# Performance work log

Measured on AMD Instinct MI355X. Metric: run time of the kernel, lower is better.

Reference implementation:

```python
import jax, jax.numpy as jnp
import numpy as np

NUM_HEADS = 12
ALPHA = 4.0
EPS = 1e-6

def safe_pow(x, p):
    # relu(x)**p with grad-safe handling of x<=0 (avoids nan from log(0) in pow grads)
    xp = jnp.where(x > 0, x, 1.0)
    return jnp.where(x > 0, xp ** p, 0.0)

def setup_inputs() -> dict:
    key = jax.random.key(0)
    ks = jax.random.split(key, 9)
    B, N, C = 8, 4096, 768
    Hn, hd, ksz = NUM_HEADS, C // NUM_HEADS, 5
    return {
        "x": jax.random.normal(ks[0], (B, N, C), jnp.float32),
        "Wqg": jax.random.normal(ks[1], (C, 2 * C), jnp.float32) * 0.02,
        "Wkv": jax.random.normal(ks[2], (C, 2 * C), jnp.float32) * 0.02,
        "Wproj": jax.random.normal(ks[3], (C, C), jnp.float32) * 0.02,
        "bproj": jnp.zeros((C,), jnp.float32),
        "dwc_w": jax.random.normal(ks[4], (hd, 1, ksz, ksz), jnp.float32) * 0.05,
        "dwc_b": jnp.zeros((hd,), jnp.float32),
        "power_p": jax.random.normal(ks[5], (1, Hn, 1, hd), jnp.float32) * 0.01,
        "scale_p": jax.random.normal(ks[6], (1, 1, C), jnp.float32) * 0.01,
        "pos_enc": jax.random.normal(ks[7], (1, N, C), jnp.float32) * 0.01,
    }

def reference(x, Wqg, Wkv, Wproj, bproj, dwc_w, dwc_b, power_p, scale_p, pos_enc):
    B, N, C = x.shape
    Hn = NUM_HEADS
    hd = C // Hn
    # q/g projection: [B,N,2C] -> q = [...,0,:], g = [...,1,:]
    qg = (x @ Wqg).reshape(B, N, 2, C)
    q, g = qg[:, :, 0], qg[:, :, 1]
    # k/v projection (sr_ratio == 1)
    kvp = x @ Wkv
    k, v = kvp[..., :C], kvp[..., C:]
    k = k + pos_enc
    scale = jax.nn.softplus(scale_p)            # [1,1,C]
    power = 1.0 + ALPHA * jax.nn.sigmoid(power_p)  # [1,Hn,1,hd]
    q = q / scale
    k = k / scale
    # -> [B,Hn,N,hd]
    q = q.reshape(B, N, Hn, hd).transpose(0, 2, 1, 3)
    k = k.reshape(B, N, Hn, hd).transpose(0, 2, 1, 3)
    v = v.reshape(B, N, Hn, hd).transpose(0, 2, 1, 3)
    q_pos = safe_pow(q, power)
    q_neg = safe_pow(-q, power)
    k_pos = safe_pow(k, power)
    k_neg = safe_pow(-k, power)
    q_sim = jnp.concatenate([q_pos, q_neg], -1)  # [B,Hn,N,2hd]
    q_opp = jnp.concatenate([q_neg, q_pos], -1)
    k_cat = jnp.concatenate([k_pos, k_neg], -1)
    v1, v2 = jnp.split(v, 2, axis=-1)            # [B,Hn,N,hd/2]
    n = N
    inv_n = 1.0 / n
    k_mean = k_cat.mean(axis=2, keepdims=True)   # [B,Hn,1,2hd]
    z_sim = 1.0 / (jnp.einsum('bhnk,bhmk->bhnm', q_sim, k_mean) + EPS)  # [B,Hn,N,1]
    kv1 = jnp.einsum('bhnk,bhnv->bhkv', k_cat, v1) * inv_n
    x_sim = jnp.einsum('bhnk,bhkv->bhnv', q_sim, kv1) * z_sim
    z_opp = 1.0 / (jnp.einsum('bhnk,bhmk->bhnm', q_opp, k_mean) + EPS)
    kv2 = jnp.einsum('bhnk,bhnv->bhkv', k_cat, v2) * inv_n
    x_opp = jnp.einsum('bhnk,bhkv->bhnv', q_opp, kv2) * z_opp
    xa = jnp.concatenate([x_sim, x_opp], -1).transpose(0, 2, 1, 3).reshape(B, N, C)
    # depthwise-conv positional branch on v (head-major channel layout)
    Hs = int(np.sqrt(N))
    v_img = v.reshape(B * Hn, Hs, Hs, hd).transpose(0, 3, 1, 2)  # [B*Hn, hd, Hs, Hs]
    v_conv = jax.lax.conv_general_dilated(
        v_img, dwc_w, (1, 1), 'SAME', feature_group_count=hd,
        dimension_numbers=('NCHW', 'OIHW', 'NCHW')) + dwc_b[None, :, None, None]
    v_pos = v_conv.reshape(B, C, N).transpose(0, 2, 1)  # [B,N,C]
    out = (xa + v_pos) * g
    return out @ Wproj + bproj
```

## Files before the change

kernel.cpp:

```cpp
#include <hip/hip_runtime.h>


typedef _Float16 f16;
typedef __attribute__((ext_vector_type(4))) float f32x4;
typedef __attribute__((ext_vector_type(8))) _Float16 f16x8;
typedef __attribute__((ext_vector_type(4))) _Float16 f16x4;

__device__ __forceinline__ void mfma(f32x4& c, f16x8 a, f16x8 b) {
  c = __builtin_amdgcn_mfma_f32_16x16x32_f16(a, b, c, 0, 0, 0);
}

__device__ __forceinline__ void gload_lds16(const f16* g, f16* l) {
  __builtin_amdgcn_global_load_lds(
      (__attribute__((address_space(1))) void*)g,
      (__attribute__((address_space(3))) void*)l, 16, 0, 0);
}

__device__ __forceinline__ f16x8 relu8(f16x8 v) {
  f16x8 r;
#pragma unroll
  for (int u = 0; u < 8; ++u) r[u] = (v[u] > (f16)0) ? v[u] : (f16)0;
  return r;
}
__device__ __forceinline__ f16x8 nrelu8(f16x8 v) {
  f16x8 r;
#pragma unroll
  for (int u = 0; u < 8; ++u) r[u] = (v[u] < (f16)0) ? (f16)(-v[u]) : (f16)0;
  return r;
}

__global__ void prep_scalars_kernel(const float* __restrict__ scale_p,
                                    const float* __restrict__ power_p,
                                    float* __restrict__ iscale,
                                    float* __restrict__ powr) {
  int c = blockIdx.x * 256 + threadIdx.x;
  if (c < 768) {
    float sp = scale_p[c];
    float s = (sp > 20.f) ? sp : log1pf(__expf(sp));
    iscale[c] = 1.f / s;
    powr[c] = 1.f + 4.f / (1.f + __expf(-power_p[c]));
  }
}

__global__ __launch_bounds__(256) void cast_x_kernel(const float* __restrict__ x,
                                                     f16* __restrict__ xblk) {
  __shared__ f16 tile[128 * 72];
  const int kb = blockIdx.x, mt = blockIdx.y, t = threadIdx.x;
  const float* xp = x + (size_t)mt * 128 * 768 + kb * 64;
#pragma unroll
  for (int it = 0; it < 8; ++it) {
    int idx = it * 256 + t;
    int row = idx >> 4, kc4 = (idx & 15) * 4;
    f32x4 v = *(const f32x4*)(xp + (size_t)row * 768 + kc4);
    f16x4 h;
    h[0] = (f16)v[0]; h[1] = (f16)v[1]; h[2] = (f16)v[2]; h[3] = (f16)v[3];
    *(f16x4*)(tile + row * 72 + kc4) = h;
  }
  __syncthreads();
  f16* op = xblk + (size_t)mt * 98304 + kb * 8192;
#pragma unroll
  for (int it = 0; it < 4; ++it) {
    int c = it * 256 + t;
    int kchunk = c >> 7, m = c & 127;
    f16x4 lo = *(const f16x4*)(tile + m * 72 + kchunk * 8);
    f16x4 hi = *(const f16x4*)(tile + m * 72 + kchunk * 8 + 4);
    *(f16x4*)(op + c * 8) = lo;
    *(f16x4*)(op + c * 8 + 4) = hi;
  }
}

__global__ __launch_bounds__(256) void transpose_w_kernel(const float* __restrict__ W,
                                                          f16* __restrict__ outblk,
                                                          int Cc, int col_off) {
  __shared__ float tile[32][33];
  const int c0 = blockIdx.x * 32, r0 = blockIdx.y * 32, t = threadIdx.x;
#pragma unroll
  for (int it = 0; it < 4; ++it) {
    int rr = it * 8 + (t >> 5), cc = t & 31;
    tile[rr][cc] = W[(size_t)(r0 + rr) * Cc + c0 + cc];
  }
  __syncthreads();
  if (t < 128) {
    int cl = t >> 2, rb = t & 3;
    int cg = col_off + c0 + cl;
    int rg = r0 + rb * 8;
    f16x4 v0, v1;
#pragma unroll
    for (int u = 0; u < 4; ++u) v0[u] = (f16)tile[rb * 8 + u][cl];
#pragma unroll
    for (int u = 0; u < 4; ++u) v1[u] = (f16)tile[rb * 8 + 4 + u][cl];
    size_t base = (size_t)(cg >> 7) * 98304 + (size_t)(rg >> 3) * 1024 +
                  (size_t)(cg & 127) * 8;
    *(f16x4*)(outblk + base) = v0;
    *(f16x4*)(outblk + base + 4) = v1;
  }
}

template <int MODE>
__global__ __launch_bounds__(256) void gemm_kernel(
    const f16* __restrict__ Ablk, const f16* __restrict__ Bblk,
    const float* __restrict__ powr, const float* __restrict__ iscale,
    const float* __restrict__ pos_enc, const float* __restrict__ bproj,
    f16* __restrict__ qpow, f16* __restrict__ gbuf, f16* __restrict__ kpow,
    f16* __restrict__ vt, float* __restrict__ outp) {
  __shared__ f16 As[8192];
  __shared__ f16 Bs[8192];
  const int t = threadIdx.x;
  const int wave = t >> 6, lane = t & 63;
  const int c16 = lane & 15, q = lane >> 4;
  const int flat = blockIdx.y * gridDim.x + blockIdx.x;
  const int chunk = (int)(gridDim.x * gridDim.y) >> 3;
  const int sw = (flat & 7) * chunk + (flat >> 3);
  const int ntile = sw % (int)gridDim.x;
  const int mtile = sw / (int)gridDim.x;
  const int mwave = (wave >> 1) * 64, nwave = (wave & 1) * 64;
  const f16* Ap = Ablk + (size_t)mtile * 98304;
  const f16* Bp = Bblk + (size_t)ntile * 98304;

  f32x4 acc[4][4];
#pragma unroll
  for (int i = 0; i < 4; ++i)
#pragma unroll
    for (int j = 0; j < 4; ++j) acc[i][j] = (f32x4){0.f, 0.f, 0.f, 0.f};

  for (int k0 = 0; k0 < 768; k0 += 64) {
#pragma unroll
    for (int r = 0; r < 4; ++r) {
      const int cl = r * 256 + t;
      const int cu = r * 256 + wave * 64;
      gload_lds16(Ap + (size_t)k0 * 128 + (size_t)cl * 8,
                  As + (size_t)cu * 8);
      gload_lds16(Bp + (size_t)k0 * 128 + (size_t)cl * 8,
                  Bs + (size_t)cu * 8);
    }
    __syncthreads();
#pragma unroll
    for (int s = 0; s < 2; ++s) {
      f16x8 af[4], bfr[4];
#pragma unroll
      for (int i = 0; i < 4; ++i) {
        af[i] = *(const f16x8*)(As + (s * 4 + q) * 1024 + (mwave + i * 16 + c16) * 8);
        bfr[i] = *(const f16x8*)(Bs + (s * 4 + q) * 1024 + (nwave + i * 16 + c16) * 8);
      }
#pragma unroll
      for (int i = 0; i < 4; ++i)
#pragma unroll
        for (int j = 0; j < 4; ++j) mfma(acc[i][j], af[i], bfr[j]);
    }
    __syncthreads();
  }

  if (MODE == 0) {
    const int sec = ntile / 6;
    const int cbase = ntile * 128 - sec * 768;
    const int b = mtile >> 5;
    const int nim0 = (mtile & 31) * 128;
#pragma unroll
    for (int i = 0; i < 4; ++i) {
      const int nloc = nim0 + mwave + i * 16 + q * 4;
#pragma unroll
      for (int j = 0; j < 4; ++j) {
        const int c = cbase + nwave + j * 16 + c16;
        const int h = c >> 6, d = c & 63;
        const int bh = b * 12 + h;
        if (sec == 0) {
          const float p = powr[c], isc = iscale[c];
          const size_t qb2 = (size_t)bh * 262144 + (size_t)(nloc >> 7) * 8192;
          const int dpo = (d >> 3) * 1024 + (d & 7);
#pragma unroll
          for (int r2 = 0; r2 < 4; ++r2) {
            float val = acc[i][j][r2] * isc;
            float av = fabsf(val);
            float e = (av > 0.f) ? exp2f(p * __log2f(av)) : 0.f;
            float s = (val > 0.f) ? e : ((val < 0.f) ? -e : 0.f);
            int mrow = (nloc + r2) & 127;
            qpow[qb2 + mrow * 8 + dpo] = (f16)s;
          }
        } else if (sec == 1) {
#pragma unroll
          for (int r2 = 0; r2 < 4; ++r2)
            gbuf[((size_t)bh * 4096 + nloc + r2) * 64 + d] = (f16)acc[i][j][r2];
        } else if (sec == 2) {
          const float p = powr[c], isc = iscale[c];
          f16x4 pk;
#pragma unroll
          for (int r2 = 0; r2 < 4; ++r2) {
            int n = nloc + r2;
            float val = (acc[i][j][r2] + pos_enc[(size_t)n * 768 + c]) * isc;
            float av = fabsf(val);
            float e = (av > 0.f) ? exp2f(p * __log2f(av)) : 0.f;
            pk[r2] = (f16)((val > 0.f) ? e : ((val < 0.f) ? -e : 0.f));
          }
          const size_t kb2 =
              (size_t)bh * 262144 + (size_t)(nloc >> 3) * 512 + (nloc & 7);
          *(f16x4*)(kpow + kb2 + (size_t)d * 8) = pk;
        } else {
          f16x4 vv4;
#pragma unroll
          for (int r2 = 0; r2 < 4; ++r2) vv4[r2] = (f16)acc[i][j][r2];
          *(f16x4*)(vt + (size_t)(bh * 64 + d) * 4096 + nloc) = vv4;
        }
      }
    }
  } else {
#pragma unroll
    for (int i = 0; i < 4; ++i) {
      const int tok0 = mtile * 128 + mwave + i * 16 + q * 4;
#pragma unroll
      for (int j = 0; j < 4; ++j) {
        const int col = ntile * 128 + nwave + j * 16 + c16;
        const float bb = bproj[col];
#pragma unroll
        for (int r2 = 0; r2 < 4; ++r2)
          outp[(size_t)(tok0 + r2) * 768 + col] = acc[i][j][r2] + bb;
      }
    }
  }
}

__global__ __launch_bounds__(256) void kv_kernel(const f16* __restrict__ kpow,
                                                 const f16* __restrict__ vt,
                                                 float* __restrict__ kvp,
                                                 float* __restrict__ ksp) {
  __shared__ f16 Ks[8192];
  __shared__ f16 Vs[4096];
  __shared__ float rp[256], rn[256];
  const int bh = blockIdx.x, split = blockIdx.y, t = threadIdx.x;
  const int wave = t >> 6, lane = t & 63;
  const int c16 = lane & 15, q = lane >> 4;
  const f16* kb = kpow + (size_t)bh * 262144;
  const f16* vb = vt + (size_t)bh * 64 * 4096;
  f32x4 acc[4][2];
#pragma unroll
  for (int i = 0; i < 4; ++i)
#pragma unroll
    for (int j = 0; j < 2; ++j) acc[i][j] = (f32x4){0.f, 0.f, 0.f, 0.f};
  float sp = 0.f, sn = 0.f;

  const int n_beg = split * 1024, n_end = n_beg + 1024;
  for (int n0 = n_beg; n0 < n_end; n0 += 64) {
    f16x8 kr[2], vr[2];
#pragma unroll
    for (int r = 0; r < 2; ++r)
      kr[r] = *(const f16x8*)(kb + (size_t)n0 * 64 + (size_t)(r * 256 + t) * 8);
#pragma unroll
    for (int r = 0; r < 2; ++r) {
      int cc = r * 256 + t;
      int vv = cc >> 3, nc = cc & 7;
      vr[r] = *(const f16x8*)(vb + (size_t)vv * 4096 + n0 + nc * 8);
    }
#pragma unroll
    for (int r = 0; r < 2; ++r)
#pragma unroll
      for (int u = 0; u < 8; ++u) {
        float f = (float)kr[r][u];
        sp += (f > 0.f) ? f : 0.f;
        sn += (f < 0.f) ? -f : 0.f;
      }
    __syncthreads();
#pragma unroll
    for (int r = 0; r < 2; ++r) {
      int cp = r * 256 + t;
      int nch = cp >> 6, d = cp & 63;
      *(f16x8*)(Ks + (size_t)(nch * 1024 + d * 8)) = relu8(kr[r]);
      *(f16x8*)(Ks + (size_t)(nch * 1024 + (d + 64) * 8)) = nrelu8(kr[r]);
    }
#pragma unroll
    for (int r = 0; r < 2; ++r) {
      int cc = r * 256 + t;
      int vv = cc >> 3, nc = cc & 7;
      *(f16x8*)(Vs + (size_t)(nc * 64 + (vv ^ nc)) * 8) = vr[r];
    }
    __syncthreads();
#pragma unroll
    for (int s = 0; s < 2; ++s) {
      f16x8 af[4], bf2[2];
#pragma unroll
      for (int i = 0; i < 4; ++i) {
        int m = i * 16 + c16, nc2 = s * 4 + q;
        af[i] = *(const f16x8*)(Vs + (nc2 * 64 + (m ^ nc2)) * 8);
      }
#pragma unroll
      for (int j = 0; j < 2; ++j)
        bf2[j] = *(const f16x8*)(Ks + ((s * 4 + q) * 128 + wave * 32 + j * 16 + c16) * 8);
#pragma unroll
      for (int i = 0; i < 4; ++i)
#pragma unroll
        for (int j = 0; j < 2; ++j) mfma(acc[i][j], af[i], bf2[j]);
    }
    __syncthreads();
  }
  float* kvb = kvp + (size_t)(bh * 4 + split) * 8192;
#pragma unroll
  for (int i = 0; i < 4; ++i)
#pragma unroll
    for (int j = 0; j < 2; ++j) {
      int kk = wave * 32 + j * 16 + c16;
      int vv0 = i * 16 + q * 4;
#pragma unroll
      for (int r2 = 0; r2 < 4; ++r2)
        kvb[(size_t)(vv0 + r2) * 128 + kk] = acc[i][j][r2];
    }
  rp[t] = sp; rn[t] = sn;
  __syncthreads();
  if (t < 64) {
    float* ko = ksp + (size_t)(bh * 4 + split) * 128;
    ko[t] = rp[t] + rp[t + 64] + rp[t + 128] + rp[t + 192];
    ko[64 + t] = rn[t] + rn[t + 64] + rn[t + 128] + rn[t + 192];
  }
}

__global__ void bx_kernel(const float* __restrict__ kvp,
                          const float* __restrict__ ksp, f16* __restrict__ bxt) {
  const int bh = blockIdx.x, kk = threadIdx.x;
  const float inv_n = 1.f / 4096.f;
  const float* kv0 = kvp + (size_t)bh * 4 * 8192;
  const float* ks0 = ksp + (size_t)bh * 4 * 128;
  f16* ob = bxt + (size_t)bh * 80 * 128;
  for (int nn = 0; nn < 32; ++nn) {
    float v = kv0[nn * 128 + kk] + kv0[8192 + nn * 128 + kk] +
              kv0[16384 + nn * 128 + kk] + kv0[24576 + nn * 128 + kk];
    ob[nn * 128 + kk] = (f16)(v * inv_n);
  }
  const int kx = kk ^ 64;
  for (int nn = 32; nn < 64; ++nn) {
    float v = kv0[nn * 128 + kx] + kv0[8192 + nn * 128 + kx] +
              kv0[16384 + nn * 128 + kx] + kv0[24576 + nn * 128 + kx];
    ob[nn * 128 + kk] = (f16)(v * inv_n);
  }
  float s0 = ks0[kk] + ks0[128 + kk] + ks0[256 + kk] + ks0[384 + kk];
  ob[64 * 128 + kk] = (f16)(s0 * inv_n);
  float s1 = ks0[kx] + ks0[128 + kx] + ks0[256 + kx] + ks0[384 + kx];
  ob[65 * 128 + kk] = (f16)(s1 * inv_n);
  for (int nn = 66; nn < 80; ++nn) ob[nn * 128 + kk] = (f16)0.f;
}

__global__ __launch_bounds__(256) void conv_kernel(const f16* __restrict__ vt,
                                                   const float* __restrict__ w,
                                                   const float* __restrict__ bias,
                                                   f16* __restrict__ vpos) {
  __shared__ float img[68 * 69];
  const int blk = blockIdx.x;
  const int d = blk & 63, bh = blk >> 6;
  const f16* src = vt + (size_t)(bh * 64 + d) * 4096;
  for (int i = threadIdx.x; i < 68 * 68; i += 256) {
    int yy = i / 68, xx = i - yy * 68;
    int y = yy - 2, x = xx - 2;
    float val = 0.f;
    if (((unsigned)y < 64u) && ((unsigned)x < 64u)) val = (float)src[y * 64 + x];
    img[yy * 69 + xx] = val;
  }
  float wr[25];
#pragma unroll
  for (int k = 0; k < 25; ++k) wr[k] = w[d * 25 + k];
  const float bb = bias[d];
  __syncthreads();
  f16* dst = vpos + (size_t)(bh * 64 + d) * 4096;
  for (int g4 = threadIdx.x; g4 < 1024; g4 += 256) {
    int y = g4 >> 4, x4 = (g4 & 15) * 4;
    float o0 = bb, o1 = bb, o2 = bb, o3 = bb;
#pragma unroll
    for (int ky = 0; ky < 5; ++ky) {
      const float* row = img + (y + ky) * 69 + x4;
      float r[8];
#pragma unroll
      for (int u = 0; u < 8; ++u) r[u] = row[u];
#pragma unroll
      for (int kx = 0; kx < 5; ++kx) {
        float wv = wr[ky * 5 + kx];
        o0 += r[kx] * wv;
        o1 += r[kx + 1] * wv;
        o2 += r[kx + 2] * wv;
        o3 += r[kx + 3] * wv;
      }
    }
    f16x4 st;
    st[0] = (f16)o0; st[1] = (f16)o1; st[2] = (f16)o2; st[3] = (f16)o3;
    *(f16x4*)(dst + y * 64 + x4) = st;
  }
}

__global__ __launch_bounds__(256) void xa_kernel(
    const f16* __restrict__ qpow, const f16* __restrict__ bxt,
    const f16* __restrict__ vpos, const f16* __restrict__ gbuf,
    f16* __restrict__ pre) {
  __shared__ f16 Qs[16384];
  __shared__ f16 Ps[64 * 134];
  __shared__ float zs[256];
  const int nb = blockIdx.x, bh = blockIdx.y;
  const int b = bh / 12, h = bh % 12;
  const int t = threadIdx.x;
  const int wave = t >> 6, lane = t & 63;
  const int c16 = lane & 15, q = lane >> 4;
  const f16* qb = qpow + (size_t)bh * 262144 + (size_t)nb * 8192;
  f16x8 qr[4];
#pragma unroll
  for (int r = 0; r < 4; ++r)
    qr[r] = *(const f16x8*)(qb + (size_t)(r * 256 + t) * 8);
#pragma unroll
  for (int r = 0; r < 4; ++r) {
    int c = r * 256 + t;
    int dch = c >> 7, row = c & 127;
    *(f16x8*)(Qs + (size_t)(dch * 1024 + row * 8)) = relu8(qr[r]);
    *(f16x8*)(Qs + (size_t)((dch + 8) * 1024 + row * 8)) = nrelu8(qr[r]);
  }
  {
    const f16* vpb = vpos + (size_t)bh * 262144 + (size_t)nb * 128;
#pragma unroll
    for (int it = 0; it < 4; ++it) {
      int idx = it * 256 + t;
      int col = idx >> 4, nc = idx & 15;
      f16x8 v = *(const f16x8*)(vpb + (size_t)col * 4096 + nc * 8);
      *(f16x8*)(Ps + col * 134 + nc * 8) = v;
    }
  }
  __syncthreads();
  f32x4 acc[2][5];
#pragma unroll
  for (int i = 0; i < 2; ++i)
#pragma unroll
    for (int j = 0; j < 5; ++j) acc[i][j] = (f32x4){0.f, 0.f, 0.f, 0.f};
  const f16* bx = bxt + (size_t)bh * 80 * 128;
#pragma unroll
  for (int s = 0; s < 4; ++s) {
    f16x8 af[2], bf5[5];
#pragma unroll
    for (int i = 0; i < 2; ++i)
      af[i] = *(const f16x8*)(Qs + ((s * 4 + q) * 1024 + (wave * 32 + i * 16 + c16) * 8));
#pragma unroll
    for (int j = 0; j < 5; ++j)
      bf5[j] = *(const f16x8*)(bx + (size_t)(j * 16 + c16) * 128 + s * 32 + q * 8);
#pragma unroll
    for (int i = 0; i < 2; ++i)
#pragma unroll
      for (int j = 0; j < 5; ++j) mfma(acc[i][j], af[i], bf5[j]);
  }
  if (c16 < 2) {
#pragma unroll
    for (int i = 0; i < 2; ++i) {
      int mloc = wave * 32 + i * 16 + q * 4;
#pragma unroll
      for (int r2 = 0; r2 < 4; ++r2) zs[(mloc + r2) * 2 + c16] = acc[i][4][r2];
    }
  }
  __syncthreads();
#pragma unroll
  for (int i = 0; i < 2; ++i) {
    const int mbase = wave * 32 + i * 16 + q * 4;
#pragma unroll
    for (int j = 0; j < 4; ++j) {
      const int col = j * 16 + c16;
      const int cch = h * 64 + col;
      const int zsel = col >> 5;
#pragma unroll
      for (int r2 = 0; r2 < 4; ++r2) {
        const int mloc = mbase + r2;
        const int n = nb * 128 + mloc;
        const float den = zs[mloc * 2 + zsel];
        const float xav = acc[i][j][r2] / (den + 1e-6f);
        const float vp = (float)Ps[col * 134 + mloc];
        const float gg = (float)gbuf[((size_t)bh * 4096 + n) * 64 + col];
        const int tok = b * 4096 + n;
        pre[(size_t)(tok >> 7) * 98304 + (size_t)(cch >> 3) * 1024 +
            (tok & 127) * 8 + (cch & 7)] = (f16)((xav + vp) * gg);
      }
    }
  }
}

extern "C" void kernel_launch(void* const* d_in, const int* in_sizes, int n_in,
                              void* d_out, int out_size, void* d_ws, size_t ws_size,
                              hipStream_t stream) {
  const float* x       = (const float*)d_in[0];
  const float* Wqg     = (const float*)d_in[1];
  const float* Wkv     = (const float*)d_in[2];
  const float* Wproj   = (const float*)d_in[3];
  const float* bproj   = (const float*)d_in[4];
  const float* dwc_w   = (const float*)d_in[5];
  const float* dwc_b   = (const float*)d_in[6];
  const float* power_p = (const float*)d_in[7];
  const float* scale_p = (const float*)d_in[8];
  const float* pos_enc = (const float*)d_in[9];
  float* outp = (float*)d_out;

  char* ws = (char*)d_ws;
  constexpr size_t o_qpow = 0;
  constexpr size_t o_kpow = 50331648;
  constexpr size_t o_vt   = 100663296;
  constexpr size_t o_gbuf = 150994944;
  constexpr size_t o_xblk = 201326592;
  constexpr size_t o_wta  = 251658240;
  constexpr size_t o_wtp  = 256376832;
  constexpr size_t o_isc  = 257556480;
  constexpr size_t o_pwr  = 257560576;
  constexpr size_t o_bxt  = 257564672;
  constexpr size_t o_ks   = 259530752;

  f16*   qpow = (f16*)(ws + o_qpow);
  f16*   kpow = (f16*)(ws + o_kpow);
  f16*   vt   = (f16*)(ws + o_vt);
  f16*   gbuf = (f16*)(ws + o_gbuf);
  f16*   xblk = (f16*)(ws + o_xblk);
  f16*   wta  = (f16*)(ws + o_wta);
  f16*   wtp  = (f16*)(ws + o_wtp);
  float* isc  = (float*)(ws + o_isc);
  float* pwr  = (float*)(ws + o_pwr);
  f16*   bxt  = (f16*)(ws + o_bxt);
  float* kvp  = (float*)(ws + o_xblk);
  float* ksp  = (float*)(ws + o_xblk + 12582912);
  f16*   vpos = kpow;
  f16*   pre  = xblk;

  prep_scalars_kernel<<<dim3(3), 256, 0, stream>>>(scale_p, power_p, isc, pwr);
  cast_x_kernel<<<dim3(12, 256), 256, 0, stream>>>(x, xblk);
  transpose_w_kernel<<<dim3(48, 24), 256, 0, stream>>>(Wqg, wta, 1536, 0);
  transpose_w_kernel<<<dim3(48, 24), 256, 0, stream>>>(Wkv, wta, 1536, 1536);
  transpose_w_kernel<<<dim3(24, 24), 256, 0, stream>>>(Wproj, wtp, 768, 0);
  gemm_kernel<0><<<dim3(24, 256), 256, 0, stream>>>(
      xblk, wta, pwr, isc, pos_enc, nullptr, qpow, gbuf, kpow, vt, nullptr);
  kv_kernel<<<dim3(96, 4), 256, 0, stream>>>(kpow, vt, kvp, ksp);
  bx_kernel<<<96, 128, 0, stream>>>(kvp, ksp, bxt);
  conv_kernel<<<6144, 256, 0, stream>>>(vt, dwc_w, dwc_b, vpos);
  xa_kernel<<<dim3(32, 96), 256, 0, stream>>>(qpow, bxt, vpos, gbuf, pre);
  gemm_kernel<1><<<dim3(6, 256), 256, 0, stream>>>(
      pre, wtp, nullptr, nullptr, nullptr, bproj, nullptr, nullptr, nullptr,
      nullptr, outp);
}
```

Baseline: 701.2 us.

## Double-buffer GEMM LDS staging with larger 512-thread tiles

Restructures both GEMM kernels to use 512-thread blocks with larger output tiles (256x256 for the QKV projection, 256x128 for the output projection). Global-to-LDS loads are double-buffered in dynamic shared memory with explicit vmcnt waits and barriers, and MFMA blocks run under raised wave priority. The aim is to overlap memory staging with matrix math and raise operand reuse per tile. In exchange it uses much more LDS (128KB/96KB), which lowers occupancy, and it drops the grid swizzle for L2 locality.

```diff
diff --git a/kernel.cpp b/kernel.cpp
--- a/kernel.cpp
+++ b/kernel.cpp
@@ -97,79 +97,119 @@
 }
 
 template <int MODE>
-__global__ __launch_bounds__(256) void gemm_kernel(
+__global__ __launch_bounds__(512) void gemm_kernel(
     const f16* __restrict__ Ablk, const f16* __restrict__ Bblk,
     const float* __restrict__ powr, const float* __restrict__ iscale,
     const float* __restrict__ pos_enc, const float* __restrict__ bproj,
     f16* __restrict__ qpow, f16* __restrict__ gbuf, f16* __restrict__ kpow,
     f16* __restrict__ vt, float* __restrict__ outp) {
-  __shared__ f16 As[8192];
-  __shared__ f16 Bs[8192];
+  constexpr int NW    = (MODE == 0) ? 4 : 2;
+  constexpr int MREP  = (MODE == 0) ? 8 : 4;
+  constexpr int BCOLT = (MODE == 0) ? 2 : 1;
+  constexpr int A_H   = 16384;
+  constexpr int STR   = A_H + BCOLT * 8192;
+  extern __shared__ f16 smem[];
   const int t = threadIdx.x;
-  const int wave = t >> 6, lane = t & 63;
+  const int wid = t >> 6, lane = t & 63;
   const int c16 = lane & 15, q = lane >> 4;
-  const int flat = blockIdx.y * gridDim.x + blockIdx.x;
-  const int chunk = (int)(gridDim.x * gridDim.y) >> 3;
-  const int sw = (flat & 7) * chunk + (flat >> 3);
-  const int ntile = sw % (int)gridDim.x;
-  const int mtile = sw / (int)gridDim.x;
-  const int mwave = (wave >> 1) * 64, nwave = (wave & 1) * 64;
-  const f16* Ap = Ablk + (size_t)mtile * 98304;
-  const f16* Bp = Bblk + (size_t)ntile * 98304;
-
-  f32x4 acc[4][4];
-#pragma unroll
-  for (int i = 0; i < 4; ++i)
+  const int mtile = blockIdx.x, ntile = blockIdx.y;
+  const int wm = wid / NW, wn = wid % NW;
+  const f16* Ap = Ablk + (size_t)mtile * 196608;
+  const f16* Bp = Bblk + (size_t)ntile * (BCOLT * 98304);
+  const int ahalf = (MODE == 0) ? wm : (wm >> 1);
+  const int rbase = (MODE == 0) ? 0 : (wm & 1) * 64;
+  const int bhalf = (MODE == 0) ? (wn >> 1) : 0;
+  const int cbase = (MODE == 0) ? (wn & 1) * 64 : wn * 64;
+
+  auto STAGE = [&](int buf, int k0) {
+    const size_t gk = (size_t)k0 * 128;
+#pragma unroll
+    for (int h = 0; h < 2; ++h)
+#pragma unroll
+      for (int r = 0; r < 2; ++r)
+        gload_lds16(Ap + h * 98304 + gk + (size_t)(r * 512 + t) * 8,
+                    smem + buf * STR + h * 8192 + (r * 512 + wid * 64) * 8);
+#pragma unroll
+    for (int h = 0; h < BCOLT; ++h)
+#pragma unroll
+      for (int r = 0; r < 2; ++r)
+        gload_lds16(Bp + h * 98304 + gk + (size_t)(r * 512 + t) * 8,
+                    smem + buf * STR + A_H + h * 8192 + (r * 512 + wid * 64) * 8);
+  };
+
+  f32x4 acc[MREP][4];
+#pragma unroll
+  for (int i = 0; i < MREP; ++i)
 #pragma unroll
     for (int j = 0; j < 4; ++j) acc[i][j] = (f32x4){0.f, 0.f, 0.f, 0.f};
 
-  for (int k0 = 0; k0 < 768; k0 += 64) {
-#pragma unroll
-    for (int r = 0; r < 4; ++r) {
-      const int cl = r * 256 + t;
-      const int cu = r * 256 + wave * 64;
-      gload_lds16(Ap + (size_t)k0 * 128 + (size_t)cl * 8,
-                  As + (size_t)cu * 8);
-      gload_lds16(Bp + (size_t)k0 * 128 + (size_t)cl * 8,
-                  Bs + (size_t)cu * 8);
-    }
-    __syncthreads();
-#pragma unroll
-    for (int s = 0; s < 2; ++s) {
-      f16x8 af[4], bfr[4];
-#pragma unroll
-      for (int i = 0; i < 4; ++i) {
-        af[i] = *(const f16x8*)(As + (s * 4 + q) * 1024 + (mwave + i * 16 + c16) * 8);
-        bfr[i] = *(const f16x8*)(Bs + (s * 4 + q) * 1024 + (nwave + i * 16 + c16) * 8);
-      }
-#pragma unroll
-      for (int i = 0; i < 4; ++i)
-#pragma unroll
-        for (int j = 0; j < 4; ++j) mfma(acc[i][j], af[i], bfr[j]);
-    }
-    __syncthreads();
+  STAGE(0, 0);
+  STAGE(1, 64);
+  if constexpr (MODE == 0) asm volatile("s_waitcnt vmcnt(8)");
+  else                     asm volatile("s_waitcnt vmcnt(6)");
+  __builtin_amdgcn_sched_barrier(0);
+  __builtin_amdgcn_s_barrier();
+  __builtin_amdgcn_sched_barrier(0);
+
+  for (int j = 0; j < 12; ++j) {
+    const int cur = j & 1;
+    const f16* A_ = smem + cur * STR + ahalf * 8192;
+    const f16* B_ = smem + cur * STR + A_H + bhalf * 8192;
+#pragma unroll
+    for (int s2 = 0; s2 < 2; ++s2) {
+      f16x8 af[MREP], bf[4];
+      const int kc = (s2 * 4 + q) * 1024;
+#pragma unroll
+      for (int mi = 0; mi < MREP; ++mi)
+        af[mi] = *(const f16x8*)(A_ + kc + (rbase + mi * 16 + c16) * 8);
+#pragma unroll
+      for (int ni = 0; ni < 4; ++ni)
+        bf[ni] = *(const f16x8*)(B_ + kc + (cbase + ni * 16 + c16) * 8);
+      __builtin_amdgcn_s_setprio(1);
+#pragma unroll
+      for (int mi = 0; mi < MREP; ++mi)
+#pragma unroll
+        for (int ni = 0; ni < 4; ++ni) mfma(acc[mi][ni], af[mi], bf[ni]);
+      __builtin_amdgcn_s_setprio(0);
+    }
+    if (j < 11) {
+      asm volatile("s_waitcnt lgkmcnt(0)");
+      __builtin_amdgcn_sched_barrier(0);
+      __builtin_amdgcn_s_barrier();
+      __builtin_amdgcn_sched_barrier(0);
+      if (j < 10) {
+        STAGE(cur, (j + 2) * 64);
+        if constexpr (MODE == 0) asm volatile("s_waitcnt vmcnt(8)");
+        else                     asm volatile("s_waitcnt vmcnt(6)");
+      } else {
+        asm volatile("s_waitcnt vmcnt(0)");
+      }
+      __builtin_amdgcn_sched_barrier(0);
+      __builtin_amdgcn_s_barrier();
+      __builtin_amdgcn_sched_barrier(0);
+    }
   }
 
   if (MODE == 0) {
-    const int sec = ntile / 6;
-    const int cbase = ntile * 128 - sec * 768;
-    const int b = mtile >> 5;
-    const int nim0 = (mtile & 31) * 128;
-#pragma unroll
-    for (int i = 0; i < 4; ++i) {
-      const int nloc = nim0 + mwave + i * 16 + q * 4;
-#pragma unroll
-      for (int j = 0; j < 4; ++j) {
-        const int c = cbase + nwave + j * 16 + c16;
-        const int h = c >> 6, d = c & 63;
+    const int sec = ntile / 3;
+    const int csb = (ntile - sec * 3) * 256;
+    const int b = mtile >> 4;
+    const int nim0 = (mtile & 15) * 256;
+#pragma unroll
+    for (int mi = 0; mi < MREP; ++mi) {
+      const int nloc = nim0 + wm * 128 + mi * 16 + q * 4;
+#pragma unroll
+      for (int ni = 0; ni < 4; ++ni) {
+        const int cs = csb + wn * 64 + ni * 16 + c16;
+        const int h = cs >> 6, d = cs & 63;
         const int bh = b * 12 + h;
         if (sec == 0) {
-          const float p = powr[c], isc = iscale[c];
+          const float p = powr[cs], isc = iscale[cs];
           const size_t qb2 = (size_t)bh * 262144 + (size_t)(nloc >> 7) * 8192;
           const int dpo = (d >> 3) * 1024 + (d & 7);
 #pragma unroll
           for (int r2 = 0; r2 < 4; ++r2) {
-            float val = acc[i][j][r2] * isc;
+            float val = acc[mi][ni][r2] * isc;
             float av = fabsf(val);
             float e = (av > 0.f) ? exp2f(p * __log2f(av)) : 0.f;
             float s = (val > 0.f) ? e : ((val < 0.f) ? -e : 0.f);
@@ -179,14 +219,14 @@
         } else if (sec == 1) {
 #pragma unroll
           for (int r2 = 0; r2 < 4; ++r2)
-            gbuf[((size_t)bh * 4096 + nloc + r2) * 64 + d] = (f16)acc[i][j][r2];
+            gbuf[((size_t)bh * 4096 + nloc + r2) * 64 + d] = (f16)acc[mi][ni][r2];
         } else if (sec == 2) {
-          const float p = powr[c], isc = iscale[c];
+          const float p = powr[cs], isc = iscale[cs];
           f16x4 pk;
 #pragma unroll
           for (int r2 = 0; r2 < 4; ++r2) {
             int n = nloc + r2;
-            float val = (acc[i][j][r2] + pos_enc[(size_t)n * 768 + c]) * isc;
+            float val = (acc[mi][ni][r2] + pos_enc[(size_t)n * 768 + cs]) * isc;
             float av = fabsf(val);
             float e = (av > 0.f) ? exp2f(p * __log2f(av)) : 0.f;
             pk[r2] = (f16)((val > 0.f) ? e : ((val < 0.f) ? -e : 0.f));
@@ -197,22 +237,22 @@
         } else {
           f16x4 vv4;
 #pragma unroll
-          for (int r2 = 0; r2 < 4; ++r2) vv4[r2] = (f16)acc[i][j][r2];
+          for (int r2 = 0; r2 < 4; ++r2) vv4[r2] = (f16)acc[mi][ni][r2];
           *(f16x4*)(vt + (size_t)(bh * 64 + d) * 4096 + nloc) = vv4;
         }
       }
     }
   } else {
 #pragma unroll
-    for (int i = 0; i < 4; ++i) {
-      const int tok0 = mtile * 128 + mwave + i * 16 + q * 4;
-#pragma unroll
-      for (int j = 0; j < 4; ++j) {
-        const int col = ntile * 128 + nwave + j * 16 + c16;
+    for (int mi = 0; mi < MREP; ++mi) {
+      const int tok0 = mtile * 256 + wm * 64 + mi * 16 + q * 4;
+#pragma unroll
+      for (int ni = 0; ni < 4; ++ni) {
+        const int col = ntile * 128 + wn * 64 + ni * 16 + c16;
         const float bb = bproj[col];
 #pragma unroll
         for (int r2 = 0; r2 < 4; ++r2)
-          outp[(size_t)(tok0 + r2) * 768 + col] = acc[i][j][r2] + bb;
+          outp[(size_t)(tok0 + r2) * 768 + col] = acc[mi][ni][r2] + bb;
       }
     }
   }
@@ -494,7 +534,6 @@
   constexpr size_t o_isc  = 257556480;
   constexpr size_t o_pwr  = 257560576;
   constexpr size_t o_bxt  = 257564672;
-  constexpr size_t o_ks   = 259530752;
 
   f16*   qpow = (f16*)(ws + o_qpow);
   f16*   kpow = (f16*)(ws + o_kpow);
@@ -516,13 +555,13 @@
   transpose_w_kernel<<<dim3(48, 24), 256, 0, stream>>>(Wqg, wta, 1536, 0);
   transpose_w_kernel<<<dim3(48, 24), 256, 0, stream>>>(Wkv, wta, 1536, 1536);
   transpose_w_kernel<<<dim3(24, 24), 256, 0, stream>>>(Wproj, wtp, 768, 0);
-  gemm_kernel<0><<<dim3(24, 256), 256, 0, stream>>>(
+  gemm_kernel<0><<<dim3(128, 12), 512, 131072, stream>>>(
       xblk, wta, pwr, isc, pos_enc, nullptr, qpow, gbuf, kpow, vt, nullptr);
   kv_kernel<<<dim3(96, 4), 256, 0, stream>>>(kpow, vt, kvp, ksp);
   bx_kernel<<<96, 128, 0, stream>>>(kvp, ksp, bxt);
   conv_kernel<<<6144, 256, 0, stream>>>(vt, dwc_w, dwc_b, vpos);
   xa_kernel<<<dim3(32, 96), 256, 0, stream>>>(qpow, bxt, vpos, gbuf, pre);
-  gemm_kernel<1><<<dim3(6, 256), 256, 0, stream>>>(
+  gemm_kernel<1><<<dim3(128, 6), 512, 98304, stream>>>(
       pre, wtp, nullptr, nullptr, nullptr, bproj, nullptr, nullptr, nullptr,
       nullptr, outp);
 }
```

New measurement: 611.1 us. 1.15x faster.
